# Performance work log

Measured on AMD Instinct MI355X. Metric: run time of the kernel, lower is better.

Reference implementation:

```python
import jax, jax.numpy as jnp
import numpy as np

VOCAB, EMB, H, TRK, L, BOUND = 50257, 1024, 1024, 1024, 256, 25

def setup_inputs() -> dict:
    key = jax.random.key(0)
    ks = jax.random.split(key, 16)
    s = 0.02
    return {
        "query_words": jax.random.normal(ks[0], (L, 1, H), jnp.float32),
        "query_vector": jax.random.normal(ks[1], (1, 1, TRK), jnp.float32),
        "decision_vector": jax.random.normal(ks[2], (1, 1, H), jnp.float32),
        "target_answer": jax.random.randint(ks[3], (BOUND, 1, 1), 0, VOCAB, jnp.int64),
        "emb_table": jax.random.normal(ks[4], (VOCAB, EMB), jnp.float32) * s,
        "gru_Wih": jax.random.normal(ks[5], (3 * H, EMB + TRK), jnp.float32) * s,
        "gru_Whh": jax.random.normal(ks[6], (3 * H, H), jnp.float32) * s,
        "gru_bih": jnp.zeros((3 * H,), jnp.float32),
        "gru_bhh": jnp.zeros((3 * H,), jnp.float32),
        "attn_Wq": jax.random.normal(ks[7], (H, H), jnp.float32) * s,
        "attn_bq": jnp.zeros((H,), jnp.float32),
        "attn_Wk": jax.random.normal(ks[8], (H, H), jnp.float32) * s,
        "attn_bk": jnp.zeros((H,), jnp.float32),
        "attn_v": jax.random.normal(ks[9], (H,), jnp.float32) * s,
        "concat_W": jax.random.normal(ks[10], (H, 2 * H), jnp.float32) * s,
        "concat_b": jnp.zeros((H,), jnp.float32),
        "out_W": jax.random.normal(ks[11], (VOCAB, H), jnp.float32) * s,
        "out_b": jnp.zeros((VOCAB,), jnp.float32),
    }


def reference(query_words, query_vector, decision_vector, target_answer,
              emb_table, gru_Wih, gru_Whh, gru_bih, gru_bhh,
              attn_Wq, attn_bq, attn_Wk, attn_bk, attn_v,
              concat_W, concat_b, out_W, out_b):
    # eval-mode: dropout = identity; tf_ratio=1 -> teacher forcing for all steps
    h_dim = decision_vector.shape[-1]
    qw = query_words[:, 0, :]                      # [L, H] encoder memory
    keys = qw @ attn_Wk.T + attn_bk                # precompute key projection once
    qv = query_vector.reshape(-1)                  # [TRK]
    h0 = decision_vector.reshape(-1)               # [H]
    ta = target_answer.reshape(-1).astype(jnp.int32)
    # input token per step: SOS (0), then teacher-forced targets
    idx_seq = jnp.concatenate([jnp.zeros((1,), jnp.int32), ta[: BOUND - 1]])

    def step(h, idx):
        x = jnp.concatenate([qv, emb_table[idx]])  # cat(query_vector, embedded)
        g = gru_Wih @ x + gru_bih                  # [3H]
        gh = gru_Whh @ h + gru_bhh                 # [3H]
        r = jax.nn.sigmoid(g[:h_dim] + gh[:h_dim])
        z = jax.nn.sigmoid(g[h_dim:2 * h_dim] + gh[h_dim:2 * h_dim])
        n = jnp.tanh(g[2 * h_dim:] + r * gh[2 * h_dim:])
        h_new = (1.0 - z) * n + z * h
        # additive (Bahdanau) attention over query_words
        e = jnp.tanh(keys + attn_Wq @ h_new + attn_bq) @ attn_v  # [L]
        w = jax.nn.softmax(e)
        ctx = w @ qw                                              # [H]
        vec = jnp.tanh(concat_W @ jnp.concatenate([h_new, ctx]) + concat_b)
        logits = out_W @ vec + out_b                              # [VOCAB]
        return h_new, jax.nn.log_softmax(logits)

    _, logps = jax.lax.scan(step, h0, idx_seq)     # [BOUND, VOCAB]
    answer = jnp.argmax(logps, axis=-1)            # greedy tokens per step
    return (answer, logps)
```

## Files before the change

### kernel.cpp

```cpp
#include <hip/hip_runtime.h>
#include <math.h>

#define VOCAB 50257
#define EMB 1024
#define HD 1024
#define TRK 1024
#define LQ 256
#define BND 25
#define SENT 0xAAAAAAAAu

typedef __attribute__((ext_vector_type(8))) short short8v;
typedef __attribute__((ext_vector_type(4))) float float4v;

__device__ __forceinline__ float wred(float s){
  #pragma unroll
  for (int m = 32; m >= 1; m >>= 1) s += __shfl_xor(s, m, 64);
  return s;
}

__global__ __launch_bounds__(256) void k_pre_keys(const float* __restrict__ Wih,
                                                  const float* __restrict__ qv,
                                                  const float* __restrict__ bih,
                                                  const int*   __restrict__ ta,
                                                  const float* __restrict__ emb,
                                                  const float* __restrict__ qw,
                                                  const float* __restrict__ Wk,
                                                  float* __restrict__ gib,
                                                  float* __restrict__ E,
                                                  float* __restrict__ part,
                                                  uint4* __restrict__ hxc){
  __shared__ float qt[64*256];
  int b = blockIdx.x, tid = threadIdx.x;
  if (b >= 1124){
    hxc[(b - 1124)*256 + tid] = make_uint4(SENT, SENT, SENT, SENT);
    return;
  }
  if (b < 768){
    int w = tid >> 6, lane = tid & 63;
    int row = b*4 + w;
    const float* a = Wih + (size_t)row*2048;
    float s = 0.f;
    #pragma unroll
    for (int e = 0; e < 4; e++){
      int k = e*256 + lane*4;
      float4 av = *(const float4*)(a + k);
      float4 qr = *(const float4*)(qv + k);
      s += av.x*qr.x + av.y*qr.y + av.z*qr.z + av.w*qr.w;
    }
    s = wred(s);
    if (lane == 0) gib[row] = s + bih[row];
    return;
  }
  if (b < 868){
    int g = (b - 768)*256 + tid;
    int t = g >> 10, i = g & 1023;
    int idx = (t == 0) ? 0 : ta[t-1];
    E[g] = emb[(size_t)idx*EMB + i];
    return;
  }
  int b2 = b - 868;
  int jb = b2 & 63;
  int ks = b2 >> 6;
  int l = tid;
  float acc[16];
  #pragma unroll
  for (int j = 0; j < 16; j++) acc[j] = 0.f;

  for (int kt = 0; kt < 4; kt++){
    int kb = ks*256 + kt*64;
    __syncthreads();
    #pragma unroll
    for (int p = 0; p < 16; p++){
      int fidx = (p*256 + tid)*4;
      int kk = fidx & 63, ll = fidx >> 6;
      float4 v = *(const float4*)(qw + (size_t)ll*1024 + kb + kk);
      qt[(kk+0)*256 + (ll ^ ((kk+0)&31))] = v.x;
      qt[(kk+1)*256 + (ll ^ ((kk+1)&31))] = v.y;
      qt[(kk+2)*256 + (ll ^ ((kk+2)&31))] = v.z;
      qt[(kk+3)*256 + (ll ^ ((kk+3)&31))] = v.w;
    }
    __syncthreads();
    #pragma unroll
    for (int s = 0; s < 4; s++){
      float qr[16];
      #pragma unroll
      for (int q = 0; q < 16; q++){
        int k = s*16 + q;
        qr[q] = qt[k*256 + (l ^ (k&31))];
      }
      #pragma unroll
      for (int j = 0; j < 16; j++){
        const float* wr = Wk + (size_t)(jb*16 + j)*1024 + kb + s*16;
        #pragma unroll
        for (int q4 = 0; q4 < 4; q4++){
          float4 wv = *(const float4*)(wr + q4*4);
          acc[j] += qr[q4*4+0]*wv.x + qr[q4*4+1]*wv.y
                  + qr[q4*4+2]*wv.z + qr[q4*4+3]*wv.w;
        }
      }
    }
  }
  #pragma unroll
  for (int j = 0; j < 16; j++)
    part[((size_t)ks*1024 + jb*16 + j)*256 + l] = acc[j];
}

template<int K, int NCH>
__global__ __launch_bounds__(256) void k_gemm_s2(const float* __restrict__ A, int lda,
                                                 const float* __restrict__ B, int ldb,
                                                 const float* __restrict__ bias,
                                                 float* __restrict__ C,
                                                 int R, int N, int act,
                                                 short* __restrict__ Bhi,
                                                 short* __restrict__ Blo){
  __shared__ float Bl[NCH*K];
  constexpr int KD4 = K/4;
  int tid = threadIdx.x, w = tid >> 6, lane = tid & 63;
  int row = blockIdx.x*4 + w;
  const float* a = A + (size_t)row*lda;
  float4 ar[K/256];
  #pragma unroll
  for (int e = 0; e < K/256; e++)
    ar[e] = *(const float4*)(a + e*256 + lane*4);
  float bs = bias[row];
  for (int c0 = 0; c0 < N; c0 += NCH){
    int nt = min(NCH, N - c0);
    __syncthreads();
    int total = nt*KD4;
    for (int i = tid; i < total; i += 256){
      int j = i/KD4, kk = i - j*KD4;
      *(float4*)&Bl[j*K + kk*4] = *(const float4*)(B + (size_t)(c0+j)*ldb + kk*4);
    }
    __syncthreads();
    for (int j = 0; j < nt; j++){
      float s = 0.f;
      #pragma unroll
      for (int e = 0; e < K/256; e++){
        float4 bv = *(const float4*)&Bl[j*K + e*256 + lane*4];
        s += ar[e].x*bv.x + ar[e].y*bv.y + ar[e].z*bv.z + ar[e].w*bv.w;
      }
      s = wred(s);
      if (lane == 0){
        float v = s + bs;
        if (act) v = tanhf(v);
        C[(size_t)(c0+j)*R + row] = v;
        if (Bhi){
          size_t idx = (size_t)(c0+j)*R + row;
          unsigned bits = __float_as_uint(v);
          Bhi[idx] = (short)(bits >> 16);
          float lo = v - __uint_as_float(bits & 0xFFFF0000u);
          Blo[idx] = (short)(__float_as_uint(lo) >> 16);
        }
      }
    }
  }
}

__global__ __launch_bounds__(512, 1) void k_gru8(const float* __restrict__ Whh,
                                                 const float* __restrict__ bhh,
                                                 const float* __restrict__ gi,
                                                 const float* __restrict__ dv,
                                                 float* __restrict__ HC,
                                                 unsigned* __restrict__ hxu){
  __shared__ float Wl[24][1024];
  __shared__ float hbuf[1024];
  __shared__ float sres[24];
  int tid = threadIdx.x, w = tid >> 6, lane = tid & 63;
  int b = blockIdx.x;
  for (int i = tid; i < 6144; i += 512){
    int r = i >> 8, c = (i & 255)*4;
    int g = r >> 3, s = r & 7;
    *(float4*)&Wl[r][c] = *(const float4*)(Whh + (size_t)(g*1024 + b*8 + s)*1024 + c);
  }
  if (tid < 256)
    *(float4*)&hbuf[tid*4] = *(const float4*)(dv + tid*4);
  __syncthreads();

  for (int t = 0; t < BND; t++){
    float g0=0,g1=0,g2=0,bb0=0,bb1=0,bb2=0,hpown=0;
    if (tid < 8){
      int i = b*8 + tid;
      const float* gg = gi + (size_t)t*3072;
      g0 = gg[i]; g1 = gg[1024+i]; g2 = gg[2048+i];
      bb0 = bhh[i]; bb1 = bhh[1024+i]; bb2 = bhh[2048+i];
      hpown = hbuf[i];
    }
    float hv[16];
    #pragma unroll
    for (int e = 0; e < 4; e++){
      float4 v = *(const float4*)&hbuf[e*256 + lane*4];
      hv[e*4]=v.x; hv[e*4+1]=v.y; hv[e*4+2]=v.z; hv[e*4+3]=v.w;
    }
    #pragma unroll
    for (int j = 0; j < 3; j++){
      int r = w*3 + j;
      float a = 0.f;
      #pragma unroll
      for (int e = 0; e < 4; e++){
        float4 v = *(const float4*)&Wl[r][e*256 + lane*4];
        a += v.x*hv[e*4] + v.y*hv[e*4+1] + v.z*hv[e*4+2] + v.w*hv[e*4+3];
      }
      a = wred(a);
      if (lane == 0) sres[r] = a;
    }
    __syncthreads();
    if (tid < 8){
      int i = b*8 + tid;
      float ghr = sres[tid]      + bb0;
      float ghz = sres[8  + tid] + bb1;
      float ghn = sres[16 + tid] + bb2;
      float rr = 1.f/(1.f + expf(-(g0 + ghr)));
      float zz = 1.f/(1.f + expf(-(g1 + ghz)));
      float nn = tanhf(g2 + rr*ghn);
      float hnew = (1.f - zz)*nn + zz*hpown;
      HC[(size_t)t*2048 + i] = hnew;
      if (t < BND-1){
        union { float f; unsigned u; } cv; cv.f = hnew;
        if (cv.u == SENT) cv.u ^= 1u;
        __hip_atomic_store(hxu + (size_t)t*2048 + b*16 + tid, cv.u,
                           __ATOMIC_RELAXED, __HIP_MEMORY_SCOPE_AGENT);
      }
    }
    if (t == BND-1) break;
    if (w < 2){
      int blk = w*64 + lane;
      const unsigned* bp = hxu + (size_t)t*2048 + blk*16;
      unsigned d[8];
      for (;;){
        bool ok = true;
        #pragma unroll
        for (int j = 0; j < 8; j++){
          d[j] = __hip_atomic_load(bp + j, __ATOMIC_RELAXED, __HIP_MEMORY_SCOPE_AGENT);
          ok = ok && (d[j] != SENT);
        }
        if (ok) break;
        __builtin_amdgcn_s_sleep(1);
      }
      #pragma unroll
      for (int j = 0; j < 8; j++)
        hbuf[blk*8 + j] = __uint_as_float(d[j]);
    }
    __syncthreads();
  }
}

__global__ __launch_bounds__(256) void k_attn1(const float* __restrict__ part,
                                               const float* __restrict__ bk,
                                               const float* __restrict__ Qt,
                                               const float* __restrict__ av,
                                               float* __restrict__ epart){
  int t = blockIdx.x, jc = blockIdx.y;
  int l = threadIdx.x;
  const float* q = Qt + (size_t)t*1024;
  int j0 = jc*32;
  float acc = 0.f;
  #pragma unroll
  for (int u = 0; u < 8; u++){
    #pragma unroll
    for (int v = 0; v < 4; v++){
      int j = j0 + u*4 + v;
      float kv = part[(size_t)j*256 + l]
               + part[(size_t)(1024+j)*256 + l]
               + part[(size_t)(2048+j)*256 + l]
               + part[(size_t)(3072+j)*256 + l]
               + bk[j];
      acc += tanhf(kv + q[j]) * av[j];
    }
  }
  epart[((size_t)t*32 + jc)*256 + l] = acc;
}

__global__ __launch_bounds__(256) void k_attn2(const float* __restrict__ epart,
                                               const float* __restrict__ qw,
                                               float* __restrict__ HC){
  __shared__ float red[256];
  __shared__ float sw[256];
  int t = blockIdx.x, half = blockIdx.y, tid = threadIdx.x;
  float e = 0.f;
  for (int jc = 0; jc < 32; jc++) e += epart[((size_t)t*32 + jc)*256 + tid];
  red[tid] = e; __syncthreads();
  for (int s = 128; s > 0; s >>= 1){
    if (tid < s) red[tid] = fmaxf(red[tid], red[tid+s]);
    __syncthreads();
  }
  float m = red[0]; __syncthreads();
  float wv = expf(e - m);
  red[tid] = wv; __syncthreads();
  for (int s = 128; s > 0; s >>= 1){
    if (tid < s) red[tid] += red[tid+s];
    __syncthreads();
  }
  float inv = 1.f/red[0];
  sw[tid] = wv*inv; __syncthreads();
  float2 c = make_float2(0.f, 0.f);
  const float* qp = qw + half*512 + tid*2;
  for (int ll = 0; ll < 256; ll++){
    float wl = sw[ll];
    float2 v = *(const float2*)(qp + (size_t)ll*1024);
    c.x += wl*v.x; c.y += wl*v.y;
  }
  *(float2*)(HC + (size_t)t*2048 + 1024 + half*512 + tid*2) = c;
}

__global__ __launch_bounds__(256, 1) void k_gemm_mfma5(const float* __restrict__ A,
                                                       const short* __restrict__ Bhi,
                                                       const short* __restrict__ Blo,
                                                       const float* __restrict__ bias,
                                                       float* __restrict__ C){
  int tid = threadIdx.x, lane = tid & 63, w = tid >> 6;
  int rlo = lane & 15, kg = lane >> 4;
  int R0 = blockIdx.x*128 + w*32;

  const float* ap[2];
  #pragma unroll
  for (int rt = 0; rt < 2; rt++){
    int row = R0 + rt*16 + rlo;
    if (row >= VOCAB) row = VOCAB-1;
    ap[rt] = A + (size_t)row*1024 + kg*8;
  }
  int t0 = rlo;
  int t1 = 16 + rlo; if (t1 > 24) t1 = 24;
  const short* bh0 = Bhi + t0*1024 + kg*8;
  const short* bl0 = Blo + t0*1024 + kg*8;
  const short* bh1 = Bhi + t1*1024 + kg*8;
  const short* bl1 = Blo + t1*1024 + kg*8;

  float4v acc[2][2];
  #pragma unroll
  for (int rt = 0; rt < 2; rt++)
    #pragma unroll
    for (int ct = 0; ct < 2; ct++)
      acc[rt][ct] = (float4v){0.f,0.f,0.f,0.f};

  short8v bhc[2], blc[2], bhn[2], bln[2];
  float4 a0c[2], a1c[2], a0n[2], a1n[2];

  bhc[0] = *(const short8v*)(bh0);
  blc[0] = *(const short8v*)(bl0);
  bhc[1] = *(const short8v*)(bh1);
  blc[1] = *(const short8v*)(bl1);
  #pragma unroll
  for (int rt = 0; rt < 2; rt++){
    a0c[rt] = *(const float4*)(ap[rt] + 0);
    a1c[rt] = *(const float4*)(ap[rt] + 4);
  }

  #pragma unroll 1
  for (int s = 0; s < 32; s++){
    if (s + 1 < 32){
      int ko = (s+1)*32;
      bhn[0] = *(const short8v*)(bh0 + ko);
      bln[0] = *(const short8v*)(bl0 + ko);
      bhn[1] = *(const short8v*)(bh1 + ko);
      bln[1] = *(const short8v*)(bl1 + ko);
      #pragma unroll
      for (int rt = 0; rt < 2; rt++){
        a0n[rt] = *(const float4*)(ap[rt] + ko);
        a1n[rt] = *(const float4*)(ap[rt] + ko + 4);
      }
    }
    #pragma unroll
    for (int rt = 0; rt < 2; rt++){
      float av[8] = {a0c[rt].x,a0c[rt].y,a0c[rt].z,a0c[rt].w,
                     a1c[rt].x,a1c[rt].y,a1c[rt].z,a1c[rt].w};
      short8v ah, al;
      #pragma unroll
      for (int j = 0; j < 8; j++){
        unsigned bits = __float_as_uint(av[j]);
        ah[j] = (short)(bits >> 16);
        float lo = av[j] - __uint_as_float(bits & 0xFFFF0000u);
        al[j] = (short)(__float_as_uint(lo) >> 16);
      }
      #pragma unroll
      for (int ct = 0; ct < 2; ct++){
        acc[rt][ct] = __builtin_amdgcn_mfma_f32_16x16x32_bf16(ah, bhc[ct], acc[rt][ct], 0, 0, 0);
        acc[rt][ct] = __builtin_amdgcn_mfma_f32_16x16x32_bf16(ah, blc[ct], acc[rt][ct], 0, 0, 0);
        acc[rt][ct] = __builtin_amdgcn_mfma_f32_16x16x32_bf16(al, bhc[ct], acc[rt][ct], 0, 0, 0);
      }
    }
    bhc[0] = bhn[0]; blc[0] = bln[0]; bhc[1] = bhn[1]; blc[1] = bln[1];
    #pragma unroll
    for (int rt = 0; rt < 2; rt++){
      a0c[rt] = a0n[rt]; a1c[rt] = a1n[rt];
    }
  }

  #pragma unroll
  for (int rt = 0; rt < 2; rt++){
    #pragma unroll
    for (int ct = 0; ct < 2; ct++){
      int t = ct*16 + rlo;
      if (t >= 25) continue;
      #pragma unroll
      for (int reg = 0; reg < 4; reg++){
        int rout = R0 + rt*16 + kg*4 + reg;
        if (rout < VOCAB)
          C[(size_t)t*VOCAB + rout] = acc[rt][ct][reg] + bias[rout];
      }
    }
  }
}

__global__ __launch_bounds__(256) void k_lstat(const float* __restrict__ C,
                                               float* __restrict__ pm,
                                               float* __restrict__ ps,
                                               int*   __restrict__ pa){
  __shared__ float sm[256], ss[256];
  __shared__ int   sa[256];
  int t = blockIdx.x, c = blockIdx.y, tid = threadIdx.x;
  int r0 = c*6283, r1 = min(r0 + 6283, VOCAB);
  const float* p = C + (size_t)t*VOCAB;
  float m = -3.4e38f, s = 0.f; int arg = r0;
  for (int r = r0 + tid; r < r1; r += 256){
    float x = p[r];
    if (x > m){ s = s*expf(m - x) + 1.f; m = x; arg = r; }
    else       s += expf(x - m);
  }
  sm[tid] = m; ss[tid] = s; sa[tid] = arg; __syncthreads();
  for (int st = 128; st > 0; st >>= 1){
    if (tid < st){
      float m1 = sm[tid], s1 = ss[tid]; int a1 = sa[tid];
      float m2 = sm[tid+st], s2 = ss[tid+st]; int a2 = sa[tid+st];
      if (m2 > m1){ sm[tid] = m2; ss[tid] = s2 + s1*expf(m1 - m2); sa[tid] = a2; }
      else if (m2 == m1){ ss[tid] = s1 + s2; sa[tid] = min(a1, a2); }
      else { ss[tid] = s1 + s2*expf(m2 - m1); }
    }
    __syncthreads();
  }
  if (tid == 0){ pm[t*8 + c] = sm[0]; ps[t*8 + c] = ss[0]; pa[t*8 + c] = sa[0]; }
}

__global__ __launch_bounds__(256) void k_lsub2(float* __restrict__ C,
                                               const float* __restrict__ pm,
                                               const float* __restrict__ ps,
                                               const int* __restrict__ pa,
                                               float* __restrict__ out){
  int t = blockIdx.y;
  float M = pm[t*8], S = ps[t*8]; int A = pa[t*8];
  #pragma unroll
  for (int c = 1; c < 8; c++){
    float m2 = pm[t*8+c], s2 = ps[t*8+c]; int a2 = pa[t*8+c];
    if (m2 > M){ S = s2 + S*expf(M - m2); M = m2; A = a2; }
    else if (m2 == M){ S += s2; A = min(A, a2); }
    else S += s2*expf(m2 - M);
  }
  float Lg = logf(S) + M;
  int r = blockIdx.x*256 + threadIdx.x;
  if (r < VOCAB) C[(size_t)t*VOCAB + r] -= Lg;
  if (blockIdx.x == 0 && threadIdx.x == 0) out[t] = (float)A;
}

extern "C" void kernel_launch(void* const* d_in, const int* in_sizes, int n_in,
                              void* d_out, int out_size, void* d_ws, size_t ws_size,
                              hipStream_t stream){
  const float* qw  = (const float*)d_in[0];
  const float* qv  = (const float*)d_in[1];
  const float* dv  = (const float*)d_in[2];
  const int*   ta  = (const int*)d_in[3];
  const float* emb = (const float*)d_in[4];
  const float* Wih = (const float*)d_in[5];
  const float* Whh = (const float*)d_in[6];
  const float* bih = (const float*)d_in[7];
  const float* bhh = (const float*)d_in[8];
  const float* Wq  = (const float*)d_in[9];
  const float* bq  = (const float*)d_in[10];
  const float* Wk  = (const float*)d_in[11];
  const float* bk  = (const float*)d_in[12];
  const float* av  = (const float*)d_in[13];
  const float* cW  = (const float*)d_in[14];
  const float* cb  = (const float*)d_in[15];
  const float* oW  = (const float*)d_in[16];
  const float* ob  = (const float*)d_in[17];
  float* out = (float*)d_out;
  float* ws  = (float*)d_ws;

  float* part  = ws;
  float* ep    = ws + 1048576;
  float* E     = ws + 1310720;
  float* gib   = ws + 1336320;
  float* gi    = ws + 1339392;
  float* HC    = ws + 1416192;
  float* Qt    = ws + 1467392;
  float* VEC   = ws + 1492992;
  unsigned* hx = (unsigned*)(ws + 1518592);
  float* pm    = ws + 1569792;
  float* ps    = ws + 1570048;
  int*   pa    = (int*)(ws + 1570304);
  short* Bhi   = (short*)(ws + 1570816);
  short* Blo   = (short*)(ws + 1583616);

  k_pre_keys<<<1174, 256, 0, stream>>>(Wih, qv, bih, ta, emb, qw, Wk, gib, E, part, (uint4*)hx);
  k_gemm_s2<1024,16><<<768, 256, 0, stream>>>(Wih + 1024, 2048, E, 1024, gib, gi, 3072, 25, 0, nullptr, nullptr);
  k_gru8<<<128, 512, 0, stream>>>(Whh, bhh, gi, dv, HC, hx);
  k_gemm_s2<1024,16><<<256, 256, 0, stream>>>(Wq, 1024, HC, 2048, bq, Qt, 1024, 25, 0, nullptr, nullptr);
  k_attn1<<<dim3(25,32), 256, 0, stream>>>(part, bk, Qt, av, ep);
  k_attn2<<<dim3(25,2), 256, 0, stream>>>(ep, qw, HC);
  k_gemm_s2<2048,8><<<256, 256, 0, stream>>>(cW, 2048, HC, 2048, cb, VEC, 1024, 25, 1, Bhi, Blo);
  k_gemm_mfma5<<<393, 256, 0, stream>>>(oW, Bhi, Blo, ob, out + 25);
  k_lstat<<<dim3(25,8), 256, 0, stream>>>(out + 25, pm, ps, pa);
  k_lsub2<<<dim3(197,25), 256, 0, stream>>>(out + 25, pm, ps, pa, out);
}
```

Before: 350.0 us.

## Fuse per-block online softmax statistics into output-projection GEMM epilogue

```diff
diff --git a/kernel.cpp b/kernel.cpp
--- a/kernel.cpp
+++ b/kernel.cpp
@@ -8,6 +8,7 @@
 #define LQ 256
 #define BND 25
 #define SENT 0xAAAAAAAAu
+#define NBLK_MFMA 393
 
 typedef __attribute__((ext_vector_type(8))) short short8v;
 typedef __attribute__((ext_vector_type(4))) float float4v;
@@ -302,11 +303,16 @@
   *(float2*)(HC + (size_t)t*2048 + 1024 + half*512 + tid*2) = c;
 }
 
-__global__ __launch_bounds__(256, 1) void k_gemm_mfma5(const float* __restrict__ A,
+__global__ __launch_bounds__(256, 1) void k_gemm_mfma6(const float* __restrict__ A,
                                                        const short* __restrict__ Bhi,
                                                        const short* __restrict__ Blo,
                                                        const float* __restrict__ bias,
-                                                       float* __restrict__ C){
+                                                       float* __restrict__ C,
+                                                       float* __restrict__ pmB,
+                                                       float* __restrict__ psB,
+                                                       int*   __restrict__ paB){
+  __shared__ float sm[2][16][16], ss[2][16][16];
+  __shared__ int   sa[2][16][16];
   int tid = threadIdx.x, lane = tid & 63, w = tid >> 6;
   int rlo = lane & 15, kg = lane >> 4;
   int R0 = blockIdx.x*128 + w*32;
@@ -385,69 +391,86 @@
     }
   }
 
-  #pragma unroll
-  for (int rt = 0; rt < 2; rt++){
-    #pragma unroll
-    for (int ct = 0; ct < 2; ct++){
-      int t = ct*16 + rlo;
-      if (t >= 25) continue;
+  int slot = w*4 + kg;
+  #pragma unroll
+  for (int ct = 0; ct < 2; ct++){
+    float lm = -3.4e38f, lsum = 0.f; int larg = 0;
+    int t = ct*16 + rlo;
+    #pragma unroll
+    for (int rt = 0; rt < 2; rt++){
       #pragma unroll
       for (int reg = 0; reg < 4; reg++){
         int rout = R0 + rt*16 + kg*4 + reg;
-        if (rout < VOCAB)
-          C[(size_t)t*VOCAB + rout] = acc[rt][ct][reg] + bias[rout];
-      }
-    }
-  }
-}
-
-__global__ __launch_bounds__(256) void k_lstat(const float* __restrict__ C,
-                                               float* __restrict__ pm,
-                                               float* __restrict__ ps,
-                                               int*   __restrict__ pa){
-  __shared__ float sm[256], ss[256];
-  __shared__ int   sa[256];
-  int t = blockIdx.x, c = blockIdx.y, tid = threadIdx.x;
-  int r0 = c*6283, r1 = min(r0 + 6283, VOCAB);
-  const float* p = C + (size_t)t*VOCAB;
-  float m = -3.4e38f, s = 0.f; int arg = r0;
-  for (int r = r0 + tid; r < r1; r += 256){
-    float x = p[r];
-    if (x > m){ s = s*expf(m - x) + 1.f; m = x; arg = r; }
-    else       s += expf(x - m);
-  }
-  sm[tid] = m; ss[tid] = s; sa[tid] = arg; __syncthreads();
-  for (int st = 128; st > 0; st >>= 1){
-    if (tid < st){
-      float m1 = sm[tid], s1 = ss[tid]; int a1 = sa[tid];
-      float m2 = sm[tid+st], s2 = ss[tid+st]; int a2 = sa[tid+st];
-      if (m2 > m1){ sm[tid] = m2; ss[tid] = s2 + s1*expf(m1 - m2); sa[tid] = a2; }
-      else if (m2 == m1){ ss[tid] = s1 + s2; sa[tid] = min(a1, a2); }
-      else { ss[tid] = s1 + s2*expf(m2 - m1); }
-    }
-    __syncthreads();
-  }
-  if (tid == 0){ pm[t*8 + c] = sm[0]; ps[t*8 + c] = ss[0]; pa[t*8 + c] = sa[0]; }
-}
-
-__global__ __launch_bounds__(256) void k_lsub2(float* __restrict__ C,
-                                               const float* __restrict__ pm,
-                                               const float* __restrict__ ps,
-                                               const int* __restrict__ pa,
+        if (t < 25 && rout < VOCAB){
+          float x = acc[rt][ct][reg] + bias[rout];
+          C[(size_t)t*VOCAB + rout] = x;
+          if (x > lm){ lsum = lsum*expf(lm - x) + 1.f; lm = x; larg = rout; }
+          else        lsum += expf(x - lm);
+        }
+      }
+    }
+    if (t < 25){
+      sm[ct][rlo][slot] = lm; ss[ct][rlo][slot] = lsum; sa[ct][rlo][slot] = larg;
+    }
+  }
+  __syncthreads();
+  if (tid < 32){
+    int ct = tid >> 4, rl = tid & 15;
+    int t = ct*16 + rl;
+    if (t < 25){
+      float M = sm[ct][rl][0], S = ss[ct][rl][0]; int A2 = sa[ct][rl][0];
+      #pragma unroll
+      for (int q = 1; q < 16; q++){
+        float m2 = sm[ct][rl][q], s2 = ss[ct][rl][q]; int a2 = sa[ct][rl][q];
+        if (m2 > M){ S = s2 + S*expf(M - m2); M = m2; A2 = a2; }
+        else if (m2 == M){ S += s2; A2 = min(A2, a2); }
+        else S += s2*expf(m2 - M);
+      }
+      pmB[(size_t)blockIdx.x*25 + t] = M;
+      psB[(size_t)blockIdx.x*25 + t] = S;
+      paB[(size_t)blockIdx.x*25 + t] = A2;
+    }
+  }
+}
+
+__global__ __launch_bounds__(256) void k_lcomb(const float* __restrict__ pmB,
+                                               const float* __restrict__ psB,
+                                               const int* __restrict__ paB,
+                                               float* __restrict__ Lg,
                                                float* __restrict__ out){
-  int t = blockIdx.y;
-  float M = pm[t*8], S = ps[t*8]; int A = pa[t*8];
-  #pragma unroll
-  for (int c = 1; c < 8; c++){
-    float m2 = pm[t*8+c], s2 = ps[t*8+c]; int a2 = pa[t*8+c];
+  __shared__ float rm[256], rs[256];
+  __shared__ int   ra[256];
+  int t = blockIdx.x, tid = threadIdx.x;
+  float M = -3.4e38f, S = 0.f; int A = 0x7fffffff;
+  for (int b = tid; b < NBLK_MFMA; b += 256){
+    float m2 = pmB[(size_t)b*25 + t], s2 = psB[(size_t)b*25 + t];
+    int a2 = paB[(size_t)b*25 + t];
     if (m2 > M){ S = s2 + S*expf(M - m2); M = m2; A = a2; }
     else if (m2 == M){ S += s2; A = min(A, a2); }
     else S += s2*expf(m2 - M);
   }
-  float Lg = logf(S) + M;
+  rm[tid] = M; rs[tid] = S; ra[tid] = A; __syncthreads();
+  for (int st = 128; st > 0; st >>= 1){
+    if (tid < st){
+      float m1 = rm[tid], s1 = rs[tid]; int a1 = ra[tid];
+      float m2 = rm[tid+st], s2 = rs[tid+st]; int a2 = ra[tid+st];
+      if (m2 > m1){ rm[tid] = m2; rs[tid] = s2 + s1*expf(m1 - m2); ra[tid] = a2; }
+      else if (m2 == m1){ rs[tid] = s1 + s2; ra[tid] = min(a1, a2); }
+      else { rs[tid] = s1 + s2*expf(m2 - m1); }
+    }
+    __syncthreads();
+  }
+  if (tid == 0){
+    Lg[t] = logf(rs[0]) + rm[0];
+    out[t] = (float)ra[0];
+  }
+}
+
+__global__ __launch_bounds__(256) void k_lsub3(float* __restrict__ C,
+                                               const float* __restrict__ Lg){
+  int t = blockIdx.y;
   int r = blockIdx.x*256 + threadIdx.x;
-  if (r < VOCAB) C[(size_t)t*VOCAB + r] -= Lg;
-  if (blockIdx.x == 0 && threadIdx.x == 0) out[t] = (float)A;
+  if (r < VOCAB) C[(size_t)t*VOCAB + r] -= Lg[t];
 }
 
 extern "C" void kernel_launch(void* const* d_in, const int* in_sizes, int n_in,
@@ -483,11 +506,12 @@
   float* Qt    = ws + 1467392;
   float* VEC   = ws + 1492992;
   unsigned* hx = (unsigned*)(ws + 1518592);
-  float* pm    = ws + 1569792;
-  float* ps    = ws + 1570048;
-  int*   pa    = (int*)(ws + 1570304);
+  float* Lg    = ws + 1569792;
   short* Bhi   = (short*)(ws + 1570816);
   short* Blo   = (short*)(ws + 1583616);
+  float* pmB   = ws + 1596416;
+  float* psB   = ws + 1606272;
+  int*   paB   = (int*)(ws + 1616128);
 
   k_pre_keys<<<1174, 256, 0, stream>>>(Wih, qv, bih, ta, emb, qw, Wk, gib, E, part, (uint4*)hx);
   k_gemm_s2<1024,16><<<768, 256, 0, stream>>>(Wih + 1024, 2048, E, 1024, gib, gi, 3072, 25, 0, nullptr, nullptr);
@@ -496,7 +520,7 @@
   k_attn1<<<dim3(25,32), 256, 0, stream>>>(part, bk, Qt, av, ep);
   k_attn2<<<dim3(25,2), 256, 0, stream>>>(ep, qw, HC);
   k_gemm_s2<2048,8><<<256, 256, 0, stream>>>(cW, 2048, HC, 2048, cb, VEC, 1024, 25, 1, Bhi, Blo);
-  k_gemm_mfma5<<<393, 256, 0, stream>>>(oW, Bhi, Blo, ob, out + 25);
-  k_lstat<<<dim3(25,8), 256, 0, stream>>>(out + 25, pm, ps, pa);
-  k_lsub2<<<dim3(197,25), 256, 0, stream>>>(out + 25, pm, ps, pa, out);
-}
+  k_gemm_mfma6<<<NBLK_MFMA, 256, 0, stream>>>(oW, Bhi, Blo, ob, out + 25, pmB, psB, paB);
+  k_lcomb<<<25, 256, 0, stream>>>(pmB, psB, paB, Lg, out);
+  k_lsub3<<<dim3(197,25), 256, 0, stream>>>(out + 25, Lg);
+}
```

New measurement: 351.6 us (median of 2 runs). No clear change (+0.5%).
